# Kernel tuning notes

Measured on AMD Instinct MI355X. Metric: run time of the kernel, lower is better.

The kernel has to match this reference:

```python
import jax, jax.numpy as jnp
import numpy as np
import math

FD_RADIUS = 2
FD_H = 0.01
GAUSS_WIN = 9
GAUSS_STD = 2.0


def _fd_kernel():
    # 4th-order central FD stencil for 2nd derivative (radius 2), scaled by 1/h^2
    k = np.array([-1/12, 4/3, -5/2, 4/3, -1/12], dtype=np.float32)
    return jnp.asarray(k / FD_H**2)


def _gauss_kernel():
    R = GAUSS_WIN // 2
    xs = np.arange(-R, R + 1, dtype=np.float64)
    c = 1.0 / (GAUSS_STD * math.sqrt(2 * math.pi))
    k = c * np.exp(-xs**2 / (2 * GAUSS_STD**2))
    k = k / k.sum()
    return jnp.asarray(k.astype(np.float32))


def setup_inputs() -> dict:
    key = jax.random.key(0)
    x = jax.random.normal(key, (8, 4, 1048576), dtype=jnp.float32)
    return {"x": x, "fd_kernel": _fd_kernel(), "gauss_kernel": _gauss_kernel()}


def _depthwise_valid(sig, k1d):
    # sig: [B, C, T]; same 1D kernel applied independently to every channel
    C = sig.shape[1]
    w = jnp.tile(k1d.reshape(1, 1, -1), (C, 1, 1))  # [C, 1, K]
    return jax.lax.conv_general_dilated(
        sig, w, window_strides=(1,), padding="VALID",
        dimension_numbers=("NCH", "OIH", "NCH"), feature_group_count=C)


def reference(x, fd_kernel, gauss_kernel):
    # Finite-difference 2nd derivative (valid conv), then Gaussian smoothing (valid conv)
    x_diff = _depthwise_valid(x, fd_kernel)          # [B, C, T-4]
    x_smooth = _depthwise_valid(x_diff, gauss_kernel)  # [B, C, T-12]
    return x_smooth
```

## Files before the change

kernel.cpp:

```cpp
#include <hip/hip_runtime.h>

#define T_IN   1048576
#define T_OUT  1048564
#define QPR    262141
#define SEGS   4
#define BPR    256
#define NROWS  32

__device__ __forceinline__ void compose13(const float* __restrict__ fd,
                                          const float* __restrict__ gs,
                                          float c[13])
{
    float f[5], g[9];
#pragma unroll
    for (int i = 0; i < 5; ++i) f[i] = fd[i];
#pragma unroll
    for (int j = 0; j < 9; ++j) g[j] = gs[j];
#pragma unroll
    for (int k = 0; k < 13; ++k) c[k] = 0.0f;
#pragma unroll
    for (int i = 0; i < 5; ++i)
#pragma unroll
        for (int j = 0; j < 9; ++j) c[i + j] = fmaf(f[i], g[j], c[i + j]);
}

__global__ __launch_bounds__(256) void pinn_fused_conv13_v3(
    const float* __restrict__ x,
    const float* __restrict__ fd,
    const float* __restrict__ gs,
    float* __restrict__ out)
{
    const int r  = blockIdx.x >> 8;
    const int b  = blockIdx.x & (BPR - 1);
    const int t  = threadIdx.x;
    const int q0 = (b << 10) + t;

    const float* __restrict__ xrow = x + (size_t)r * T_IN;
    float*       __restrict__ orow = out + (size_t)r * T_OUT;

    float4 v[SEGS][4];
#pragma unroll
    for (int s = 0; s < SEGS; ++s) {
        const int q = q0 + (s << 8);
        if (q < QPR) {
            const float* p = xrow + (q << 2);
#pragma unroll
            for (int i = 0; i < 4; ++i)
                v[s][i] = *reinterpret_cast<const float4*>(p + 4 * i);
        } else {
#pragma unroll
            for (int i = 0; i < 4; ++i)
                v[s][i] = make_float4(0.f, 0.f, 0.f, 0.f);
        }
    }

    float c[13];
    compose13(fd, gs, c);

#pragma unroll
    for (int s = 0; s < SEGS; ++s) {
        const int q = q0 + (s << 8);
        if (q < QPR) {
            const float a[16] = {
                v[s][0].x, v[s][0].y, v[s][0].z, v[s][0].w,
                v[s][1].x, v[s][1].y, v[s][1].z, v[s][1].w,
                v[s][2].x, v[s][2].y, v[s][2].z, v[s][2].w,
                v[s][3].x, v[s][3].y, v[s][3].z, v[s][3].w};
            float4 ov;
            float* op = &ov.x;
#pragma unroll
            for (int j = 0; j < 4; ++j) {
                float sacc = c[0] * a[j];
#pragma unroll
                for (int k = 1; k < 13; ++k) sacc = fmaf(c[k], a[j + k], sacc);
                op[j] = sacc;
            }
            *reinterpret_cast<float4*>(orow + (q << 2)) = ov;
        }
    }
}

extern "C" void kernel_launch(void* const* d_in, const int* in_sizes, int n_in,
                              void* d_out, int out_size, void* d_ws, size_t ws_size,
                              hipStream_t stream) {
    const float* x  = (const float*)d_in[0];
    const float* fd = (const float*)d_in[1];
    const float* gs = (const float*)d_in[2];
    float* out = (float*)d_out;

    pinn_fused_conv13_v3<<<NROWS * BPR, 256, 0, stream>>>(x, fd, gs, out);
}
```

Baseline: 260.1 us.

## Use persistent grid-stride loop with register double-buffered loads and nontemporal stores

Replaces the one-shot grid (256 blocks per row, 4 segments per thread) with 64 blocks per row that loop 16 times over row chunks. Each iteration double-buffers register loads, prefetching the next quad while computing and storing the current one. Output stores become nontemporal to reduce cache pollution. The aim is better latency hiding with fewer blocks, at the cost of fewer loads in flight per thread compared with the prior all-loads-first scheme.

```diff
diff --git a/kernel.cpp b/kernel.cpp
--- a/kernel.cpp
+++ b/kernel.cpp
@@ -3,9 +3,12 @@
 #define T_IN   1048576
 #define T_OUT  1048564
 #define QPR    262141
-#define SEGS   4
-#define BPR    256
 #define NROWS  32
+#define BLKROW 64
+#define SLOTS  (BLKROW * 256)
+#define NIT    16
+
+typedef float v4f __attribute__((ext_vector_type(4)));
 
 __device__ __forceinline__ void compose13(const float* __restrict__ fd,
                                           const float* __restrict__ gs,
@@ -24,60 +27,64 @@
         for (int j = 0; j < 9; ++j) c[i + j] = fmaf(f[i], g[j], c[i + j]);
 }
 
-__global__ __launch_bounds__(256) void pinn_fused_conv13_v3(
+__global__ __launch_bounds__(256) void pinn_fused_conv13_v4(
     const float* __restrict__ x,
     const float* __restrict__ fd,
     const float* __restrict__ gs,
     float* __restrict__ out)
 {
-    const int r  = blockIdx.x >> 8;
-    const int b  = blockIdx.x & (BPR - 1);
-    const int t  = threadIdx.x;
-    const int q0 = (b << 10) + t;
+    const int r = blockIdx.y;
+    const int t = threadIdx.x;
+    int q = (blockIdx.x << 8) + t;
 
     const float* __restrict__ xrow = x + (size_t)r * T_IN;
     float*       __restrict__ orow = out + (size_t)r * T_OUT;
 
-    float4 v[SEGS][4];
-#pragma unroll
-    for (int s = 0; s < SEGS; ++s) {
-        const int q = q0 + (s << 8);
-        if (q < QPR) {
-            const float* p = xrow + (q << 2);
-#pragma unroll
-            for (int i = 0; i < 4; ++i)
-                v[s][i] = *reinterpret_cast<const float4*>(p + 4 * i);
-        } else {
-#pragma unroll
-            for (int i = 0; i < 4; ++i)
-                v[s][i] = make_float4(0.f, 0.f, 0.f, 0.f);
-        }
-    }
-
     float c[13];
     compose13(fd, gs, c);
 
-#pragma unroll
-    for (int s = 0; s < SEGS; ++s) {
-        const int q = q0 + (s << 8);
-        if (q < QPR) {
-            const float a[16] = {
-                v[s][0].x, v[s][0].y, v[s][0].z, v[s][0].w,
-                v[s][1].x, v[s][1].y, v[s][1].z, v[s][1].w,
-                v[s][2].x, v[s][2].y, v[s][2].z, v[s][2].w,
-                v[s][3].x, v[s][3].y, v[s][3].z, v[s][3].w};
-            float4 ov;
-            float* op = &ov.x;
-#pragma unroll
-            for (int j = 0; j < 4; ++j) {
-                float sacc = c[0] * a[j];
-#pragma unroll
-                for (int k = 1; k < 13; ++k) sacc = fmaf(c[k], a[j + k], sacc);
-                op[j] = sacc;
-            }
-            *reinterpret_cast<float4*>(orow + (q << 2)) = ov;
-        }
+    v4f A0, A1, A2, A3, B0, B1, B2, B3;
+
+#define LOADQ(R0, R1, R2, R3, Q) do {                                   \
+        if ((Q) < QPR) {                                                \
+            const float* _p = xrow + ((size_t)(Q) << 2);                \
+            R0 = *reinterpret_cast<const v4f*>(_p);                     \
+            R1 = *reinterpret_cast<const v4f*>(_p + 4);                 \
+            R2 = *reinterpret_cast<const v4f*>(_p + 8);                 \
+            R3 = *reinterpret_cast<const v4f*>(_p + 12);                \
+        } } while (0)
+
+#define CSTORE(R0, R1, R2, R3, Q) do {                                  \
+        if ((Q) < QPR) {                                                \
+            const float a[16] = {R0.x, R0.y, R0.z, R0.w,                \
+                                 R1.x, R1.y, R1.z, R1.w,                \
+                                 R2.x, R2.y, R2.z, R2.w,                \
+                                 R3.x, R3.y, R3.z, R3.w};               \
+            v4f ov;                                                     \
+            _Pragma("unroll")                                           \
+            for (int j = 0; j < 4; ++j) {                               \
+                float s = c[0] * a[j];                                  \
+                _Pragma("unroll")                                       \
+                for (int k = 1; k < 13; ++k) s = fmaf(c[k], a[j+k], s); \
+                ov[j] = s;                                              \
+            }                                                           \
+            __builtin_nontemporal_store(ov,                             \
+                reinterpret_cast<v4f*>(orow + ((size_t)(Q) << 2)));     \
+        } } while (0)
+
+    LOADQ(A0, A1, A2, A3, q);
+
+#pragma unroll 1
+    for (int i = 0; i < NIT / 2; ++i) {
+        LOADQ (B0, B1, B2, B3, q + SLOTS);
+        CSTORE(A0, A1, A2, A3, q);
+        LOADQ (A0, A1, A2, A3, q + 2 * SLOTS);
+        CSTORE(B0, B1, B2, B3, q + SLOTS);
+        q += 2 * SLOTS;
     }
+
+#undef LOADQ
+#undef CSTORE
 }
 
 extern "C" void kernel_launch(void* const* d_in, const int* in_sizes, int n_in,
@@ -88,5 +95,6 @@
     const float* gs = (const float*)d_in[2];
     float* out = (float*)d_out;
 
-    pinn_fused_conv13_v3<<<NROWS * BPR, 256, 0, stream>>>(x, fd, gs, out);
+    dim3 grid(BLKROW, NROWS);
+    pinn_fused_conv13_v4<<<grid, 256, 0, stream>>>(x, fd, gs, out);
 }
```

After: 249.3 us. -4.2%, faster.
